# Optimization experiments

Hardware: AMD Instinct MI355X
Metric: run time of the kernel (lower is better)

Reference implementation:

```python
import jax, jax.numpy as jnp
import numpy as np

LN_EPS = 1e-6


def setup_inputs() -> dict:
    key = jax.random.key(0)
    ks = jax.random.split(key, 8)
    B, T, V, r, c, D = 1, 2048, 50257, 16, 16, 1024
    rc = r * c
    return {
        "input_ids": jax.random.randint(ks[0], (B, T), 0, V),
        "token_to_mu_w": jax.random.normal(ks[1], (rc, V), jnp.float32) * 0.02,  # nn.Linear(V, rc).weight
        "pos_embedding": jax.random.normal(ks[2], (1, T, r, c), jnp.float32) * 0.02,
        "w1": jax.random.normal(ks[3], (D, rc), jnp.float32) * 0.05,  # Linear(rc, D).weight
        "b1": jnp.zeros((D,), jnp.float32),
        "ln_w": jnp.ones((D,), jnp.float32),
        "ln_b": jnp.zeros((D,), jnp.float32),
        "w2": jax.random.normal(ks[4], (V, D), jnp.float32) * 0.02,  # Linear(D, V).weight
        "b2": jnp.zeros((V,), jnp.float32),
    }


def reference(input_ids, token_to_mu_w, pos_embedding, w1, b1, ln_w, ln_b, w2, b2):
    B, T = input_ids.shape
    r, c = pos_embedding.shape[2], pos_embedding.shape[3]
    # one_hot(input_ids) @ W^T is exactly a row-gather of W^T (single nonzero per row)
    MU = jnp.take(token_to_mu_w.T, input_ids, axis=0)          # [B, T, rc]
    MU = MU.reshape(B, T, r, c) + pos_embedding[:, :T]         # [B, T, r, c]
    # n_layers = 0: no transformer blocks; dropout is identity in eval
    x = MU.reshape(B, T, r * c)
    h = jax.nn.gelu(jnp.einsum('btk,dk->btd', x, w1) + b1, approximate=False)
    mean = jnp.mean(h, axis=-1, keepdims=True)
    var = jnp.mean(jnp.square(h - mean), axis=-1, keepdims=True)
    h = (h - mean) * jax.lax.rsqrt(var + LN_EPS) * ln_w + ln_b
    logits = jnp.einsum('btd,vd->btv', h, w2) + b2             # [B, T, V]
    return logits, MU
```

## Files before the change

### kernel.cpp

```cpp
#include <hip/hip_runtime.h>
#include <hip/hip_bf16.h>
#include <math.h>

#define T_LEN 2048
#define RC 256
#define DIM 1024
#define VOCAB 50257
#define NT2 16
#define SLOTW 16384
#define HALFW 8192

using short8  = __attribute__((ext_vector_type(8))) short;
using f32x4   = __attribute__((ext_vector_type(4))) float;

#define VMCNT(n) asm volatile("s_waitcnt vmcnt(" #n ")" ::: "memory")
#define LGKM0()  asm volatile("s_waitcnt lgkmcnt(0)" ::: "memory")
#define SCHED_FENCE() __builtin_amdgcn_sched_barrier(0)

__device__ __forceinline__ unsigned short f2bf(float f) {
    unsigned int u = __float_as_uint(f);
    u += 0x7fffu + ((u >> 16) & 1u);
    return (unsigned short)(u >> 16);
}

__device__ __forceinline__ unsigned int cvt_pk_bf16(float a, float b) {
    unsigned int r;
    asm volatile("v_cvt_pk_bf16_f32 %0, %1, %2" : "=v"(r) : "v"(a), "v"(b));
    return r;
}

__device__ __forceinline__ void async_load16(void* lds, const void* g) {
    __builtin_amdgcn_global_load_lds(
        (const __attribute__((address_space(1))) void*)g,
        (__attribute__((address_space(3))) void*)lds,
        16, 0, 0);
}

__global__ __launch_bounds__(256) void mu_kernel(
    const int* __restrict__ ids, const float* __restrict__ tokw,
    const float* __restrict__ pos, float* __restrict__ mu) {
    int t = blockIdx.x, k = threadIdx.x;
    int id = ids[t];
    float v = tokw[(size_t)k * VOCAB + id] + pos[t * RC + k];
    mu[t * RC + k] = v;
}

__global__ __launch_bounds__(256) void gemm1_gelu_kernel(
    const float* __restrict__ mu, const float* __restrict__ w1,
    const float* __restrict__ b1, float* __restrict__ hpre) {
    __shared__ float xs[16][RC];
    const int tg = blockIdx.x, ng = blockIdx.y, tid = threadIdx.x;
    const int t0 = tg * 16;
    {
        const float4* src = (const float4*)(mu + (size_t)t0 * RC);
        float4* dst = (float4*)&xs[0][0];
        #pragma unroll
        for (int i = 0; i < 4; ++i) dst[tid + 256 * i] = src[tid + 256 * i];
    }
    __syncthreads();
    const int d = ng * 256 + tid;
    float acc[16];
    const float bias = b1[d];
    #pragma unroll
    for (int t = 0; t < 16; ++t) acc[t] = bias;
    const float4* w1r = (const float4*)(w1 + (size_t)d * RC);
    for (int k4 = 0; k4 < RC / 4; ++k4) {
        const float4 w = w1r[k4];
        #pragma unroll
        for (int t = 0; t < 16; ++t) {
            const float4 xv = *(const float4*)&xs[t][k4 * 4];
            acc[t] += w.x * xv.x + w.y * xv.y + w.z * xv.z + w.w * xv.w;
        }
    }
    #pragma unroll
    for (int t = 0; t < 16; ++t) {
        float x = acc[t];
        float g = 0.5f * x * (1.0f + erff(x * 0.70710678118654752f));
        hpre[(size_t)(t0 + t) * DIM + d] = g;
    }
}

__global__ __launch_bounds__(256) void ln_kernel(
    const float* __restrict__ hpre, const float* __restrict__ lnw,
    const float* __restrict__ lnb, unsigned short* __restrict__ h) {
    const int t = blockIdx.x, tid = threadIdx.x;
    const float4 v = ((const float4*)(hpre + (size_t)t * DIM))[tid];
    float s  = v.x + v.y + v.z + v.w;
    float ss = v.x * v.x + v.y * v.y + v.z * v.z + v.w * v.w;
    #pragma unroll
    for (int off = 32; off > 0; off >>= 1) {
        s  += __shfl_down(s, off, 64);
        ss += __shfl_down(ss, off, 64);
    }
    __shared__ float red[8];
    const int wid = tid >> 6, lane = tid & 63;
    if (lane == 0) { red[wid] = s; red[4 + wid] = ss; }
    __syncthreads();
    const float S  = red[0] + red[1] + red[2] + red[3];
    const float SS = red[4] + red[5] + red[6] + red[7];
    const float mean = S * (1.0f / DIM);
    const float var  = SS * (1.0f / DIM) - mean * mean;
    const float inv  = 1.0f / sqrtf(var + 1e-6f);
    const float4 wv = ((const float4*)lnw)[tid];
    const float4 bv = ((const float4*)lnb)[tid];
    ushort4 o;
    o.x = f2bf((v.x - mean) * inv * wv.x + bv.x);
    o.y = f2bf((v.y - mean) * inv * wv.y + bv.y);
    o.z = f2bf((v.z - mean) * inv * wv.z + bv.z);
    o.w = f2bf((v.w - mean) * inv * wv.w + bv.w);
    ((ushort4*)h)[(size_t)t * (DIM / 4) + tid] = o;
}

__global__ __launch_bounds__(256) void cvt_kernel(
    const float* __restrict__ src, unsigned int* __restrict__ dst, int n8) {
    int i = blockIdx.x * 256 + threadIdx.x;
    const int stride = gridDim.x * 256;
    for (; i < n8; i += stride) {
        const float4 a = ((const float4*)src)[2 * i];
        const float4 b = ((const float4*)src)[2 * i + 1];
        uint4 o;
        o.x = cvt_pk_bf16(a.x, a.y);
        o.y = cvt_pk_bf16(a.z, a.w);
        o.z = cvt_pk_bf16(b.x, b.y);
        o.w = cvt_pk_bf16(b.z, b.w);
        ((uint4*)dst)[i] = o;
    }
}

__device__ __forceinline__ void stage_halfA(
    const unsigned short* __restrict__ A, unsigned short* dst,
    int m0, int half, int kt, int tid) {
    #pragma unroll
    for (int p = 0; p < 2; ++p) {
        const int idx = p * 512 + tid;
        const int r   = idx >> 3;
        const int gl  = (idx & 7) ^ (r & 7);
        async_load16(dst + (size_t)idx * 8,
                     A + (size_t)(m0 + half * 128 + r) * DIM + kt * 64 + gl * 8);
    }
}
__device__ __forceinline__ void stage_halfB(
    const unsigned short* __restrict__ B, unsigned short* dst,
    int n0, int half, int kt, int tid) {
    #pragma unroll
    for (int p = 0; p < 2; ++p) {
        const int idx = p * 512 + tid;
        const int r   = idx >> 3;
        const int gl  = (idx & 7) ^ (r & 7);
        int row = n0 + half * 128 + r; if (row > VOCAB - 1) row = VOCAB - 1;
        async_load16(dst + (size_t)idx * 8,
                     B + (size_t)row * DIM + kt * 64 + gl * 8);
    }
}

__global__ __launch_bounds__(512, 1) void gemm2_kernel(
    const unsigned short* __restrict__ A, const unsigned short* __restrict__ B,
    const float* __restrict__ b2, float* __restrict__ out) {
    __shared__ unsigned short As[2 * SLOTW];
    __shared__ unsigned short Bs[2 * SLOTW];

    const int tid  = threadIdx.x;
    const int cpx  = gridDim.x >> 3;
    const int wgid = (blockIdx.x & 7) * cpx + (blockIdx.x >> 3);
    const int m0   = (wgid & 7) << 8;
    const int n0   = (wgid >> 3) << 8;

    const int lane = tid & 63;
    const int lr   = lane & 15;
    const int lk   = lane >> 4;
    const int wid  = tid >> 6;
    const int wr   = wid >> 2;
    const int wc   = wid & 3;
    const int sx   = lr & 7;

    f32x4 acc[8][4];
    #pragma unroll
    for (int m = 0; m < 8; ++m)
        #pragma unroll
        for (int n = 0; n < 4; ++n) acc[m][n] = {0.f, 0.f, 0.f, 0.f};

    stage_halfB(B, Bs,                 n0, 0, 0, tid);
    stage_halfB(B, Bs + HALFW,         n0, 1, 0, tid);
    stage_halfA(A, As,                 m0, 0, 0, tid);
    stage_halfA(A, As + HALFW,         m0, 1, 0, tid);
    stage_halfB(B, Bs + SLOTW,         n0, 0, 1, tid);
    stage_halfB(B, Bs + SLOTW + HALFW, n0, 1, 1, tid);
    stage_halfA(A, As + SLOTW,         m0, 0, 1, tid);
    VMCNT(6);
    __builtin_amdgcn_s_barrier();

    short8 af[8], bfr[8];

    #pragma unroll 1
    for (int k = 0; k < NT2; ++k) {
        const unsigned short* As_t = As + (k & 1) * SLOTW;
        const unsigned short* Bs_t = Bs + (k & 1) * SLOTW;
        unsigned short* As_n  = As + ((k + 1) & 1) * SLOTW;
        unsigned short* As_n2 = As + (k & 1) * SLOTW;
        unsigned short* Bs_n2 = Bs + (k & 1) * SLOTW;

        #pragma unroll
        for (int mi = 0; mi < 4; ++mi) {
            const int R = wr * 128 + mi * 16 + lr;
            #pragma unroll
            for (int kk = 0; kk < 2; ++kk)
                af[mi * 2 + kk] =
                    *(const short8*)(As_t + R * 64 + (((kk * 4 + lk) ^ sx) << 3));
        }
        #pragma unroll
        for (int ni = 0; ni < 4; ++ni) {
            const int R = wc * 64 + ni * 16 + lr;
            #pragma unroll
            for (int kk = 0; kk < 2; ++kk)
                bfr[ni * 2 + kk] =
                    *(const short8*)(Bs_t + R * 64 + (((kk * 4 + lk) ^ sx) << 3));
        }
        if (k + 1 < NT2) stage_halfA(A, As_n + HALFW, m0, 1, k + 1, tid);
        __builtin_amdgcn_s_barrier();
        LGKM0();
        SCHED_FENCE();
        __builtin_amdgcn_s_setprio(1);
        #pragma unroll
        for (int mi = 0; mi < 4; ++mi)
            #pragma unroll
            for (int ni = 0; ni < 2; ++ni)
                #pragma unroll
                for (int kk = 0; kk < 2; ++kk)
                    acc[mi][ni] = __builtin_amdgcn_mfma_f32_16x16x32_bf16(
                        af[mi * 2 + kk], bfr[ni * 2 + kk], acc[mi][ni], 0, 0, 0);
        __builtin_amdgcn_s_setprio(0);
        __builtin_amdgcn_s_barrier();

        if (k + 2 < NT2) stage_halfB(B, Bs_n2, n0, 0, k + 2, tid);
        __builtin_amdgcn_s_setprio(1);
        #pragma unroll
        for (int mi = 0; mi < 4; ++mi)
            #pragma unroll
            for (int ni = 2; ni < 4; ++ni)
                #pragma unroll
                for (int kk = 0; kk < 2; ++kk)
                    acc[mi][ni] = __builtin_amdgcn_mfma_f32_16x16x32_bf16(
                        af[mi * 2 + kk], bfr[ni * 2 + kk], acc[mi][ni], 0, 0, 0);
        __builtin_amdgcn_s_setprio(0);
        __builtin_amdgcn_s_barrier();

        #pragma unroll
        for (int mi = 0; mi < 4; ++mi) {
            const int R = wr * 128 + (mi + 4) * 16 + lr;
            #pragma unroll
            for (int kk = 0; kk < 2; ++kk)
                af[mi * 2 + kk] =
                    *(const short8*)(As_t + R * 64 + (((kk * 4 + lk) ^ sx) << 3));
        }
        if (k + 2 < NT2) stage_halfB(B, Bs_n2 + HALFW, n0, 1, k + 2, tid);
        __builtin_amdgcn_s_barrier();
        LGKM0();
        SCHED_FENCE();
        __builtin_amdgcn_s_setprio(1);
        #pragma unroll
        for (int mi = 0; mi < 4; ++mi)
            #pragma unroll
            for (int ni = 0; ni < 2; ++ni)
                #pragma unroll
                for (int kk = 0; kk < 2; ++kk)
                    acc[mi + 4][ni] = __builtin_amdgcn_mfma_f32_16x16x32_bf16(
                        af[mi * 2 + kk], bfr[ni * 2 + kk], acc[mi + 4][ni], 0, 0, 0);
        __builtin_amdgcn_s_setprio(0);
        __builtin_amdgcn_s_barrier();

        if (k + 2 < NT2) stage_halfA(A, As_n2, m0, 0, k + 2, tid);
        __builtin_amdgcn_s_setprio(1);
        #pragma unroll
        for (int mi = 0; mi < 4; ++mi)
            #pragma unroll
            for (int ni = 2; ni < 4; ++ni)
                #pragma unroll
                for (int kk = 0; kk < 2; ++kk)
                    acc[mi + 4][ni] = __builtin_amdgcn_mfma_f32_16x16x32_bf16(
                        af[mi * 2 + kk], bfr[ni * 2 + kk], acc[mi + 4][ni], 0, 0, 0);
        __builtin_amdgcn_s_setprio(0);
        if (k < NT2 - 2)       { VMCNT(6); }
        else if (k == NT2 - 2) { VMCNT(0); }
        __builtin_amdgcn_s_barrier();
    }

    float bias[4]; int col[4]; bool ok[4];
    #pragma unroll
    for (int n = 0; n < 4; ++n) {
        col[n] = n0 + wc * 64 + n * 16 + lr;
        ok[n]  = col[n] < VOCAB;
        bias[n] = ok[n] ? b2[col[n]] : 0.f;
    }
    #pragma unroll
    for (int m = 0; m < 8; ++m) {
        const int row = m0 + wr * 128 + m * 16 + lk * 4;
        #pragma unroll
        for (int n = 0; n < 4; ++n) {
            if (ok[n]) {
                #pragma unroll
                for (int j = 0; j < 4; ++j)
                    out[(size_t)(row + j) * VOCAB + col[n]] = acc[m][n][j] + bias[n];
            }
        }
    }
}

extern "C" void kernel_launch(void* const* d_in, const int* in_sizes, int n_in,
                              void* d_out, int out_size, void* d_ws, size_t ws_size,
                              hipStream_t stream) {
    (void)in_sizes; (void)n_in; (void)out_size; (void)ws_size;
    const int*   ids  = (const int*)d_in[0];
    const float* tokw = (const float*)d_in[1];
    const float* pos  = (const float*)d_in[2];
    const float* w1   = (const float*)d_in[3];
    const float* b1   = (const float*)d_in[4];
    const float* lnw  = (const float*)d_in[5];
    const float* lnb  = (const float*)d_in[6];
    const float* w2   = (const float*)d_in[7];
    const float* b2   = (const float*)d_in[8];

    float* logits = (float*)d_out;
    float* mu_out = logits + (size_t)T_LEN * VOCAB;

    unsigned short* w2b = (unsigned short*)d_ws;
    unsigned short* hb  = (unsigned short*)((char*)d_ws + (size_t)VOCAB * DIM * 2);
    float* hpre = logits;

    mu_kernel<<<dim3(T_LEN), dim3(256), 0, stream>>>(ids, tokw, pos, mu_out);
    gemm1_gelu_kernel<<<dim3(T_LEN / 16, DIM / 256), dim3(256), 0, stream>>>(
        mu_out, w1, b1, hpre);
    ln_kernel<<<dim3(T_LEN), dim3(256), 0, stream>>>(hpre, lnw, lnb, hb);
    cvt_kernel<<<dim3(2048), dim3(256), 0, stream>>>(
        w2, (unsigned int*)w2b, (int)((size_t)VOCAB * DIM / 8));
    const int ntiles_n = (VOCAB + 255) / 256;
    gemm2_kernel<<<dim3(8 * ntiles_n), dim3(512), 0, stream>>>(hb, w2b, b2, logits);
}
```

Measured before the change: 482.4 us.

## Restructure GEMM main loop into split-fragment register pipeline with partial lgkm waits

The output GEMM's K loop is reorganised so A and B register fragments are split into low/high halves and loaded just ahead of the MFMA quadrant that uses them. Next-tile fragments are prefetched during the last quadrant, and the full lgkmcnt(0) waits become partial ones. The A/B async staging schedule is also reshuffled, with A staged one step ahead and B two steps ahead, and the prologue wait is adjusted to match. The aim is to hide LDS read latency behind MFMAs and remove barrier stalls. In exchange it raises register pressure and depends on fragile hand-counted waitcnt values.

```diff
diff --git a/kernel.cpp b/kernel.cpp
--- a/kernel.cpp
+++ b/kernel.cpp
@@ -14,7 +14,7 @@
 using f32x4   = __attribute__((ext_vector_type(4))) float;
 
 #define VMCNT(n) asm volatile("s_waitcnt vmcnt(" #n ")" ::: "memory")
-#define LGKM0()  asm volatile("s_waitcnt lgkmcnt(0)" ::: "memory")
+#define LGKM(n)  asm volatile("s_waitcnt lgkmcnt(" #n ")" ::: "memory")
 #define SCHED_FENCE() __builtin_amdgcn_sched_barrier(0)
 
 __device__ __forceinline__ unsigned short f2bf(float f) {
@@ -185,39 +185,46 @@
     stage_halfA(A, As + HALFW,         m0, 1, 0, tid);
     stage_halfB(B, Bs + SLOTW,         n0, 0, 1, tid);
     stage_halfB(B, Bs + SLOTW + HALFW, n0, 1, 1, tid);
-    stage_halfA(A, As + SLOTW,         m0, 0, 1, tid);
-    VMCNT(6);
+    VMCNT(4);
     __builtin_amdgcn_s_barrier();
 
-    short8 af[8], bfr[8];
+    short8 afL[8], afH[8], bfL[4], bfH[4];
+    #pragma unroll
+    for (int mi = 0; mi < 4; ++mi) {
+        const int R = wr * 128 + mi * 16 + lr;
+        #pragma unroll
+        for (int kk = 0; kk < 2; ++kk)
+            afL[mi * 2 + kk] =
+                *(const short8*)(As + R * 64 + (((kk * 4 + lk) ^ sx) << 3));
+    }
+    #pragma unroll
+    for (int ni = 0; ni < 2; ++ni) {
+        const int R = wc * 64 + ni * 16 + lr;
+        #pragma unroll
+        for (int kk = 0; kk < 2; ++kk)
+            bfL[ni * 2 + kk] =
+                *(const short8*)(Bs + R * 64 + (((kk * 4 + lk) ^ sx) << 3));
+    }
 
     #pragma unroll 1
-    for (int k = 0; k < NT2; ++k) {
-        const unsigned short* As_t = As + (k & 1) * SLOTW;
-        const unsigned short* Bs_t = Bs + (k & 1) * SLOTW;
-        unsigned short* As_n  = As + ((k + 1) & 1) * SLOTW;
-        unsigned short* As_n2 = As + (k & 1) * SLOTW;
-        unsigned short* Bs_n2 = Bs + (k & 1) * SLOTW;
-
-        #pragma unroll
-        for (int mi = 0; mi < 4; ++mi) {
-            const int R = wr * 128 + mi * 16 + lr;
+    for (int j = 0; j < NT2; ++j) {
+        const unsigned short* As_t = As + (j & 1) * SLOTW;
+        const unsigned short* Bs_t = Bs + (j & 1) * SLOTW;
+        const unsigned short* As_n = As + ((j + 1) & 1) * SLOTW;
+        const unsigned short* Bs_n = Bs + ((j + 1) & 1) * SLOTW;
+        unsigned short* As_w  = As + ((j + 1) & 1) * SLOTW;
+        unsigned short* Bs_w2 = Bs + (j & 1) * SLOTW;
+
+        #pragma unroll
+        for (int ni = 0; ni < 2; ++ni) {
+            const int R = wc * 64 + (ni + 2) * 16 + lr;
             #pragma unroll
             for (int kk = 0; kk < 2; ++kk)
-                af[mi * 2 + kk] =
-                    *(const short8*)(As_t + R * 64 + (((kk * 4 + lk) ^ sx) << 3));
-        }
-        #pragma unroll
-        for (int ni = 0; ni < 4; ++ni) {
-            const int R = wc * 64 + ni * 16 + lr;
-            #pragma unroll
-            for (int kk = 0; kk < 2; ++kk)
-                bfr[ni * 2 + kk] =
+                bfH[ni * 2 + kk] =
                     *(const short8*)(Bs_t + R * 64 + (((kk * 4 + lk) ^ sx) << 3));
         }
-        if (k + 1 < NT2) stage_halfA(A, As_n + HALFW, m0, 1, k + 1, tid);
-        __builtin_amdgcn_s_barrier();
-        LGKM0();
+        if (j + 1 < NT2) stage_halfA(A, As_w, m0, 0, j + 1, tid);
+        LGKM(4);
         SCHED_FENCE();
         __builtin_amdgcn_s_setprio(1);
         #pragma unroll
@@ -227,11 +234,21 @@
                 #pragma unroll
                 for (int kk = 0; kk < 2; ++kk)
                     acc[mi][ni] = __builtin_amdgcn_mfma_f32_16x16x32_bf16(
-                        af[mi * 2 + kk], bfr[ni * 2 + kk], acc[mi][ni], 0, 0, 0);
+                        afL[mi * 2 + kk], bfL[ni * 2 + kk], acc[mi][ni], 0, 0, 0);
         __builtin_amdgcn_s_setprio(0);
         __builtin_amdgcn_s_barrier();
 
-        if (k + 2 < NT2) stage_halfB(B, Bs_n2, n0, 0, k + 2, tid);
+        #pragma unroll
+        for (int mi = 0; mi < 4; ++mi) {
+            const int R = wr * 128 + (mi + 4) * 16 + lr;
+            #pragma unroll
+            for (int kk = 0; kk < 2; ++kk)
+                afH[mi * 2 + kk] =
+                    *(const short8*)(As_t + R * 64 + (((kk * 4 + lk) ^ sx) << 3));
+        }
+        if (j + 1 < NT2) stage_halfA(A, As_w + HALFW, m0, 1, j + 1, tid);
+        LGKM(8);
+        SCHED_FENCE();
         __builtin_amdgcn_s_setprio(1);
         #pragma unroll
         for (int mi = 0; mi < 4; ++mi)
@@ -240,21 +257,12 @@
                 #pragma unroll
                 for (int kk = 0; kk < 2; ++kk)
                     acc[mi][ni] = __builtin_amdgcn_mfma_f32_16x16x32_bf16(
-                        af[mi * 2 + kk], bfr[ni * 2 + kk], acc[mi][ni], 0, 0, 0);
+                        afL[mi * 2 + kk], bfH[(ni - 2) * 2 + kk], acc[mi][ni], 0, 0, 0);
         __builtin_amdgcn_s_setprio(0);
         __builtin_amdgcn_s_barrier();
 
-        #pragma unroll
-        for (int mi = 0; mi < 4; ++mi) {
-            const int R = wr * 128 + (mi + 4) * 16 + lr;
-            #pragma unroll
-            for (int kk = 0; kk < 2; ++kk)
-                af[mi * 2 + kk] =
-                    *(const short8*)(As_t + R * 64 + (((kk * 4 + lk) ^ sx) << 3));
-        }
-        if (k + 2 < NT2) stage_halfB(B, Bs_n2 + HALFW, n0, 1, k + 2, tid);
-        __builtin_amdgcn_s_barrier();
-        LGKM0();
+        if (j + 2 < NT2) stage_halfB(B, Bs_w2, n0, 0, j + 2, tid);
+        LGKM(0);
         SCHED_FENCE();
         __builtin_amdgcn_s_setprio(1);
         #pragma unroll
@@ -264,11 +272,35 @@
                 #pragma unroll
                 for (int kk = 0; kk < 2; ++kk)
                     acc[mi + 4][ni] = __builtin_amdgcn_mfma_f32_16x16x32_bf16(
-                        af[mi * 2 + kk], bfr[ni * 2 + kk], acc[mi + 4][ni], 0, 0, 0);
+                        afH[mi * 2 + kk], bfL[ni * 2 + kk], acc[mi + 4][ni], 0, 0, 0);
         __builtin_amdgcn_s_setprio(0);
         __builtin_amdgcn_s_barrier();
 
-        if (k + 2 < NT2) stage_halfA(A, As_n2, m0, 0, k + 2, tid);
+        if (j + 2 < NT2) stage_halfB(B, Bs_w2 + HALFW, n0, 1, j + 2, tid);
+        if (j + 2 < NT2)      { VMCNT(4); }
+        else if (j + 1 < NT2) { VMCNT(0); }
+        if (j + 1 < NT2) {
+            #pragma unroll
+            for (int ni = 0; ni < 2; ++ni) {
+                const int R = wc * 64 + ni * 16 + lr;
+                #pragma unroll
+                for (int kk = 0; kk < 2; ++kk)
+                    bfL[ni * 2 + kk] =
+                        *(const short8*)(Bs_n + R * 64 + (((kk * 4 + lk) ^ sx) << 3));
+            }
+            #pragma unroll
+            for (int mi = 0; mi < 4; ++mi) {
+                const int R = wr * 128 + mi * 16 + lr;
+                #pragma unroll
+                for (int kk = 0; kk < 2; ++kk)
+                    afL[mi * 2 + kk] =
+                        *(const short8*)(As_n + R * 64 + (((kk * 4 + lk) ^ sx) << 3));
+            }
+            LGKM(12);
+        } else {
+            LGKM(0);
+        }
+        SCHED_FENCE();
         __builtin_amdgcn_s_setprio(1);
         #pragma unroll
         for (int mi = 0; mi < 4; ++mi)
@@ -277,10 +309,8 @@
                 #pragma unroll
                 for (int kk = 0; kk < 2; ++kk)
                     acc[mi + 4][ni] = __builtin_amdgcn_mfma_f32_16x16x32_bf16(
-                        af[mi * 2 + kk], bfr[ni * 2 + kk], acc[mi + 4][ni], 0, 0, 0);
+                        afH[mi * 2 + kk], bfH[(ni - 2) * 2 + kk], acc[mi + 4][ni], 0, 0, 0);
         __builtin_amdgcn_s_setprio(0);
-        if (k < NT2 - 2)       { VMCNT(6); }
-        else if (k == NT2 - 2) { VMCNT(0); }
         __builtin_amdgcn_s_barrier();
     }
 
@@ -298,8 +328,8 @@
         for (int n = 0; n < 4; ++n) {
             if (ok[n]) {
                 #pragma unroll
-                for (int j = 0; j < 4; ++j)
-                    out[(size_t)(row + j) * VOCAB + col[n]] = acc[m][n][j] + bias[n];
+                for (int jj = 0; jj < 4; ++jj)
+                    out[(size_t)(row + jj) * VOCAB + col[n]] = acc[m][n][jj] + bias[n];
             }
         }
     }
```

Measured after the change: 983.0 us. +103.8%, slower.
